# Kernel tuning notes

Hardware: AMD Instinct MI355X
Metric: run time of the kernel (lower is better)

## Reference

```python
import jax, jax.numpy as jnp
import numpy as np

N_NODES = 100000
N_EDGES = 1600000
NODE_IN = 6
EDGE_IN = 4
HID = 128


def _glorot(key, shape):
    fan_in, fan_out = shape[0], shape[1]
    lim = (6.0 / (fan_in + fan_out)) ** 0.5
    return jax.random.uniform(key, shape, jnp.float32, -lim, lim)


def setup_inputs() -> dict:
    key = jax.random.key(0)
    ks = jax.random.split(key, 16)
    x = jax.random.normal(ks[0], (N_NODES, NODE_IN), jnp.float32)
    edge_index = jax.random.randint(ks[1], (2, N_EDGES), 0, N_NODES, jnp.int64)
    edge_attr = jax.random.normal(ks[2], (N_EDGES, EDGE_IN), jnp.float32)
    # SAGEConv params: out = x @ W_root + mean_neigh @ W_neigh + b
    params = {
        "w1_root": _glorot(ks[3], (NODE_IN, HID)),
        "w1_neigh": _glorot(ks[4], (NODE_IN, HID)),
        "b1": jnp.zeros((HID,), jnp.float32),
        "w2_root": _glorot(ks[5], (HID, HID)),
        "w2_neigh": _glorot(ks[6], (HID, HID)),
        "b2": jnp.zeros((HID,), jnp.float32),
        "w_e1": _glorot(ks[7], (2 * HID + EDGE_IN, HID)),
        "b_e1": jnp.zeros((HID,), jnp.float32),
        "w_e2": _glorot(ks[8], (HID, HID // 2)),
        "b_e2": jnp.zeros((HID // 2,), jnp.float32),
        "w_e3": _glorot(ks[9], (HID // 2, 1)),
        "b_e3": jnp.zeros((1,), jnp.float32),
    }
    return {"x": x, "edge_index": edge_index, "edge_attr": edge_attr, **params}


def _sage(x, src, dst, w_root, w_neigh, b):
    # mean aggregation of source features into destination nodes
    agg = jax.ops.segment_sum(x[src], dst, num_segments=N_NODES)
    cnt = jax.ops.segment_sum(jnp.ones((src.shape[0], 1), x.dtype), dst, num_segments=N_NODES)
    mean = agg / jnp.maximum(cnt, 1.0)
    return x @ w_root + mean @ w_neigh + b


def reference(x, edge_index, edge_attr,
              w1_root, w1_neigh, b1, w2_root, w2_neigh, b2,
              w_e1, b_e1, w_e2, b_e2, w_e3, b_e3):
    src, dst = edge_index[0], edge_index[1]
    h = jax.nn.relu(_sage(x, src, dst, w1_root, w1_neigh, b1))
    # dropout is identity in eval mode
    h = jax.nn.relu(_sage(h, src, dst, w2_root, w2_neigh, b2))
    # per-edge representation: [h[src], h[dst], edge_attr] -> MLP -> scalar
    e = jnp.concatenate([h[src], h[dst], edge_attr], axis=-1)  # [E, 2H+Ein]
    e = jax.nn.relu(e @ w_e1 + b_e1)
    e = jax.nn.relu(e @ w_e2 + b_e2)
    out = (e @ w_e3 + b_e3).squeeze(-1)  # [E]
    return out
```

## Files before the change

kernel.cpp:

```cpp
#include <hip/hip_runtime.h>
#include <hip/hip_bf16.h>
#include <stdint.h>


typedef unsigned short u16;
typedef short bf16x8 __attribute__((ext_vector_type(8)));
typedef float f32x4 __attribute__((ext_vector_type(4)));

#define NMASK 0x1FFFF

__device__ __forceinline__ u16 f2b(float f) {
  unsigned u = __builtin_bit_cast(unsigned, f);
  u = u + 0x7fffu + ((u >> 16) & 1u);
  return (u16)(u >> 16);
}
__device__ __forceinline__ float bflo(unsigned u) {
  return __builtin_bit_cast(float, u << 16);
}
__device__ __forceinline__ float bfhi(unsigned u) {
  return __builtin_bit_cast(float, u & 0xffff0000u);
}
__device__ __forceinline__ unsigned pack2bf(float a, float b) {
  unsigned ua = __builtin_bit_cast(unsigned, a);
  unsigned ub = __builtin_bit_cast(unsigned, b);
  ua = ua + 0x7fffu + ((ua >> 16) & 1u);
  ub = ub + 0x7fffu + ((ub >> 16) & 1u);
  return (ua >> 16) | (ub & 0xffff0000u);
}

__global__ void hist_kernel(const int* __restrict__ ei, int* __restrict__ cnt,
                            int E) {
  int e = blockIdx.x * blockDim.x + threadIdx.x;
  if (e < E) atomicAdd(&cnt[ei[E + e]], 1);
}

__global__ void scan_block_sums(const int* __restrict__ cnt,
                                int* __restrict__ partial, int N) {
  __shared__ int red[256];
  int t = threadIdx.x;
  int n = blockIdx.x * 256 + t;
  red[t] = (n < N) ? cnt[n] : 0;
  __syncthreads();
  for (int off = 128; off; off >>= 1) {
    if (t < off) red[t] += red[t + off];
    __syncthreads();
  }
  if (t == 0) partial[blockIdx.x] = red[0];
}

__global__ void scan_partials(int* __restrict__ partial,
                              int* __restrict__ rowptr, int NBLK, int E,
                              int N) {
  __shared__ int sc[512];
  int t = threadIdx.x;
  int v = (t < NBLK) ? partial[t] : 0;
  sc[t] = v;
  __syncthreads();
  for (int off = 1; off < 512; off <<= 1) {
    int a = (t >= off) ? sc[t - off] : 0;
    __syncthreads();
    sc[t] += a;
    __syncthreads();
  }
  if (t < NBLK) partial[t] = sc[t] - v;
  if (t == 0) rowptr[N] = E;
}

__global__ void scan_final(const int* __restrict__ partial,
                           int* __restrict__ cursor, int* __restrict__ rowptr,
                           int N) {
  __shared__ int sc[256];
  int t = threadIdx.x;
  int n = blockIdx.x * 256 + t;
  int v = (n < N) ? cursor[n] : 0;
  sc[t] = v;
  __syncthreads();
  for (int off = 1; off < 256; off <<= 1) {
    int a = (t >= off) ? sc[t - off] : 0;
    __syncthreads();
    sc[t] += a;
    __syncthreads();
  }
  int excl = partial[blockIdx.x] + sc[t] - v;
  if (n < N) {
    rowptr[n] = excl;
    cursor[n] = excl;
  }
}

__global__ void scatter_csr(const int* __restrict__ ei,
                            int* __restrict__ cursor, uint2* __restrict__ csr2,
                            int E) {
  int e = blockIdx.x * blockDim.x + threadIdx.x;
  if (e >= E) return;
  int s = ei[e];
  int d = ei[E + e];
  int pos = atomicAdd(&cursor[d], 1);
  unsigned long long v = (unsigned long long)(unsigned)s |
                         ((unsigned long long)(unsigned)d << 17) |
                         ((unsigned long long)(unsigned)e << 34);
  csr2[pos] = make_uint2((unsigned)v, (unsigned)(v >> 32));
}

__global__ void permute_attr(const float* __restrict__ attr,
                             const uint2* __restrict__ csr2,
                             float4* __restrict__ attrp, int E) {
  int i = blockIdx.x * 256 + threadIdx.x;
  if (i >= E) return;
  uint2 pk = csr2[i];
  int eid = (int)((((unsigned long long)pk.y << 32) | pk.x) >> 34);
  attrp[i] = *(const float4*)(attr + (size_t)eid * 4);
}

__global__ void pack_weights(const float* __restrict__ w2_root,
                             const float* __restrict__ w2_neigh,
                             const float* __restrict__ w_e1,
                             const float* __restrict__ w_e2,
                             const float* __restrict__ b_e1,
                             u16* __restrict__ B2f, u16* __restrict__ WSDf,
                             u16* __restrict__ W2f, float* __restrict__ pbias) {
  int t = blockIdx.x * 256 + threadIdx.x;
  if (t < 32768) {
    int j = t & 7, lane = (t >> 3) & 63, nt = (t >> 9) & 7, kt = t >> 12;
    int k = kt * 32 + (lane >> 4) * 8 + j;
    int n = nt * 16 + (lane & 15);
    float v = (k < 128) ? w2_root[k * 128 + n] : w2_neigh[(k - 128) * 128 + n];
    B2f[t] = f2b(v);
  } else if (t < 65536) {
    int t2 = t - 32768;
    int j = t2 & 7, lane = (t2 >> 3) & 63, nt = (t2 >> 9) & 15, kt = t2 >> 13;
    int k = kt * 32 + (lane >> 4) * 8 + j;
    int n = nt * 16 + (lane & 15);
    float v = (n < 128) ? w_e1[k * 128 + n] : w_e1[(128 + k) * 128 + (n - 128)];
    WSDf[t2] = f2b(v);
  } else if (t < 73728) {
    int t2 = t - 65536;
    int j = t2 & 7, lane = (t2 >> 3) & 63, nt = (t2 >> 9) & 3, kt = t2 >> 11;
    int k = kt * 32 + (lane >> 4) * 8 + j;
    int n = nt * 16 + (lane & 15);
    W2f[t2] = f2b(w_e2[k * 64 + n]);
  } else if (t < 73984) {
    int n = t - 73728;
    pbias[n] = (n < 128) ? 0.0f : b_e1[n - 128];
  }
}

__global__ __launch_bounds__(256) void agg1_kernel(
    const float* __restrict__ x, const int* __restrict__ rowptr,
    const uint2* __restrict__ csr2, float* __restrict__ mean1, int N) {
  int n = blockIdx.x * 4 + (threadIdx.x >> 6);
  if (n >= N) return;
  int lane = threadIdx.x & 63;
  int g = lane >> 3;
  int c = lane & 7;
  int beg = rowptr[n], end = rowptr[n + 1];
  float a = 0.0f;
  if (c < 6) {
    for (int i = beg + g; i < end; i += 8) {
      int s = (int)(csr2[i].x & NMASK);
      a += x[(size_t)s * 6 + c];
    }
  }
  a += __shfl_xor(a, 8, 64);
  a += __shfl_xor(a, 16, 64);
  a += __shfl_xor(a, 32, 64);
  if (g == 0 && c < 6)
    mean1[(size_t)n * 6 + c] = a / (float)max(end - beg, 1);
}

__global__ void dense1_kernel(const float* __restrict__ x,
                              const float* __restrict__ mean1,
                              const float* __restrict__ w_root,
                              const float* __restrict__ w_neigh,
                              const float* __restrict__ b,
                              u16* __restrict__ cat2b, int N) {
  int n = blockIdx.x;
  int m = threadIdx.x;
  if (n >= N) return;
  float s = b[m];
#pragma unroll
  for (int j = 0; j < 6; j++) {
    s += x[(size_t)n * 6 + j] * w_root[j * 128 + m] +
         mean1[(size_t)n * 6 + j] * w_neigh[j * 128 + m];
  }
  cat2b[(size_t)n * 256 + m] = f2b(fmaxf(s, 0.0f));
}

__global__ __launch_bounds__(256) void agg2_kernel(
    const u16* __restrict__ cat2b, u16* __restrict__ cat2w,
    const int* __restrict__ rowptr, const uint2* __restrict__ csr2, int N) {
  int n = blockIdx.x * 4 + (threadIdx.x >> 6);
  if (n >= N) return;
  int lane = threadIdx.x & 63;
  int g = lane >> 4;
  int c = lane & 15;
  int beg = rowptr[n], end = rowptr[n + 1];
  float acc[8];
#pragma unroll
  for (int j = 0; j < 8; j++) acc[j] = 0.0f;
  for (int i = beg + g; i < end; i += 4) {
    int s = (int)(csr2[i].x & NMASK);
    uint4 u = *(const uint4*)(cat2b + (size_t)s * 256 + c * 8);
    acc[0] += bflo(u.x); acc[1] += bfhi(u.x);
    acc[2] += bflo(u.y); acc[3] += bfhi(u.y);
    acc[4] += bflo(u.z); acc[5] += bfhi(u.z);
    acc[6] += bflo(u.w); acc[7] += bfhi(u.w);
  }
#pragma unroll
  for (int j = 0; j < 8; j++) {
    acc[j] += __shfl_xor(acc[j], 16, 64);
    acc[j] += __shfl_xor(acc[j], 32, 64);
  }
  if (g == 0) {
    float inv = 1.0f / (float)max(end - beg, 1);
    uint4 ov;
    ov.x = pack2bf(acc[0] * inv, acc[1] * inv);
    ov.y = pack2bf(acc[2] * inv, acc[3] * inv);
    ov.z = pack2bf(acc[4] * inv, acc[5] * inv);
    ov.w = pack2bf(acc[6] * inv, acc[7] * inv);
    *(uint4*)(cat2w + (size_t)n * 256 + 128 + c * 8) = ov;
  }
}

template <int KT, int NT, bool RELU>
__global__ __launch_bounds__(256) void mfma_gemm(
    const u16* __restrict__ A, int lda, const u16* __restrict__ Bf,
    const float* __restrict__ bias, u16* __restrict__ C, int ldc, int M) {
  __shared__ u16 sB[KT * NT * 512];
  int tid = threadIdx.x;
  for (int i = tid; i < KT * NT * 64; i += 256)
    ((uint4*)sB)[i] = ((const uint4*)Bf)[i];
  int w = tid >> 6, l = tid & 63;
  int quad = l >> 4, col16 = l & 15;
  int rowA = blockIdx.x * 64 + w * 16 + col16;
  bool rv = rowA < M;
  const u16* ap = A + (size_t)rowA * lda + quad * 8;
  f32x4 acc[NT];
#pragma unroll
  for (int nt = 0; nt < NT; nt++) acc[nt] = (f32x4){0.f, 0.f, 0.f, 0.f};
  __syncthreads();
#pragma unroll
  for (int kt = 0; kt < KT; kt++) {
    bf16x8 av = {};
    if (rv) av = *(const bf16x8*)(ap + kt * 32);
#pragma unroll
    for (int nt = 0; nt < NT; nt++) {
      bf16x8 bv = *(const bf16x8*)(sB + ((kt * NT + nt) * 64 + l) * 8);
      acc[nt] = __builtin_amdgcn_mfma_f32_16x16x32_bf16(av, bv, acc[nt], 0, 0, 0);
    }
  }
  int rowbase = blockIdx.x * 64 + w * 16 + quad * 4;
#pragma unroll
  for (int r = 0; r < 4; r++) {
    int row = rowbase + r;
    if (row < M) {
#pragma unroll
      for (int nt = 0; nt < NT; nt++) {
        float v = acc[nt][r] + bias[nt * 16 + col16];
        if (RELU) v = fmaxf(v, 0.0f);
        C[(size_t)row * ldc + nt * 16 + col16] = f2b(v);
      }
    }
  }
}

__global__ __launch_bounds__(256) void edge_mfma_kernel(
    const u16* __restrict__ Pcatb, const uint2* __restrict__ csr2,
    const float4* __restrict__ attrp, const float* __restrict__ w_e1,
    const u16* __restrict__ W2f, const float* __restrict__ b_e2,
    const float* __restrict__ w_e3, const float* __restrict__ b_e3,
    float* __restrict__ out, int E) {
  __shared__ u16 sV[2][64 * 136];
  __shared__ u16 sW2[8192];

  int tid = threadIdx.x;
  int w = tid >> 6, l = tid & 63, quad = l >> 4, c16 = l & 15;
  int egrp = tid >> 4, ac16 = tid & 15;

  for (int i = tid; i < 1024; i += 256)
    ((uint4*)sW2)[i] = ((const uint4*)W2f)[i];

  float wa[4][8];
#pragma unroll
  for (int j = 0; j < 4; j++) {
    *(float4*)&wa[j][0] = *(const float4*)(w_e1 + (256 + j) * 128 + ac16 * 8);
    *(float4*)&wa[j][4] = *(const float4*)(w_e1 + (256 + j) * 128 + ac16 * 8 + 4);
  }
  float w3v[4], be2[4];
#pragma unroll
  for (int nt = 0; nt < 4; nt++) {
    w3v[nt] = w_e3[nt * 16 + c16];
    be2[nt] = b_e2[nt * 16 + c16];
  }
  float b3 = b_e3[0];

  int tiles = (E + 63) >> 6;
  int S = gridDim.x;

  uint2 pk[4];
  uint4 ps[4], pd[4];
  float4 at[4];
  int eidr[4];

  auto load_pk = [&](int t) {
#pragma unroll
    for (int it = 0; it < 4; it++) {
      int e = min(t * 64 + it * 16 + egrp, E - 1);
      pk[it] = csr2[e];
    }
  };
  auto issue_gather = [&](int t) {
#pragma unroll
    for (int it = 0; it < 4; it++) {
      unsigned long long v =
          ((unsigned long long)pk[it].y << 32) | pk[it].x;
      int s = (int)(v & NMASK);
      int d = (int)((v >> 17) & NMASK);
      eidr[it] = (int)(v >> 34);
      ps[it] = *(const uint4*)(Pcatb + (size_t)s * 256 + ac16 * 8);
      pd[it] = *(const uint4*)(Pcatb + (size_t)d * 256 + 128 + ac16 * 8);
      int e = min(t * 64 + it * 16 + egrp, E - 1);
      at[it] = attrp[e];
    }
  };

  int t = blockIdx.x;
  if (t < tiles) {
    load_pk(t);
    issue_gather(t);
    if (t + S < tiles) load_pk(t + S);
  }
  int buf = 0;
  for (; t < tiles; t += S) {
    u16* sv = sV[buf];
#pragma unroll
    for (int it = 0; it < 4; it++) {
      int e = it * 16 + egrp;
      uint4 psu = ps[it], pdu = pd[it];
      float4 a4 = at[it];
      unsigned pu[4] = {psu.x, psu.y, psu.z, psu.w};
      unsigned du[4] = {pdu.x, pdu.y, pdu.z, pdu.w};
      uint4 ov;
      unsigned* op = (unsigned*)&ov;
#pragma unroll
      for (int p2 = 0; p2 < 4; p2++) {
        int t0 = p2 * 2, t1 = t0 + 1;
        float f0 = bflo(pu[p2]) + bflo(du[p2]) + a4.x * wa[0][t0] +
                   a4.y * wa[1][t0] + a4.z * wa[2][t0] + a4.w * wa[3][t0];
        float f1 = bfhi(pu[p2]) + bfhi(du[p2]) + a4.x * wa[0][t1] +
                   a4.y * wa[1][t1] + a4.z * wa[2][t1] + a4.w * wa[3][t1];
        op[p2] = pack2bf(fmaxf(f0, 0.0f), fmaxf(f1, 0.0f));
      }
      *(uint4*)(sv + e * 136 + ac16 * 8) = ov;
      if (ac16 == 0) *(unsigned*)(sv + e * 136 + 128) = (unsigned)eidr[it];
    }
    if (t + S < tiles) {
      issue_gather(t + S);
      if (t + 2 * S < tiles) load_pk(t + 2 * S);
    }
    __syncthreads();
    f32x4 acc[4];
#pragma unroll
    for (int nt = 0; nt < 4; nt++) acc[nt] = (f32x4){0.f, 0.f, 0.f, 0.f};
    const u16* vp = sv + (w * 16 + c16) * 136 + quad * 8;
#pragma unroll
    for (int kt = 0; kt < 4; kt++) {
      bf16x8 av = *(const bf16x8*)(vp + kt * 32);
#pragma unroll
      for (int nt = 0; nt < 4; nt++) {
        bf16x8 bv = *(const bf16x8*)(sW2 + ((kt * 4 + nt) * 64 + l) * 8);
        acc[nt] = __builtin_amdgcn_mfma_f32_16x16x32_bf16(av, bv, acc[nt], 0, 0, 0);
      }
    }
#pragma unroll
    for (int r = 0; r < 4; r++) {
      float p = 0.0f;
#pragma unroll
      for (int nt = 0; nt < 4; nt++)
        p += fmaxf(acc[nt][r] + be2[nt], 0.0f) * w3v[nt];
      p += __shfl_xor(p, 1, 64);
      p += __shfl_xor(p, 2, 64);
      p += __shfl_xor(p, 4, 64);
      p += __shfl_xor(p, 8, 64);
      if (c16 == 0) {
        int eloc = w * 16 + quad * 4 + r;
        if (t * 64 + eloc < E) {
          unsigned eid = *(const unsigned*)(sv + eloc * 136 + 128);
          out[eid] = p + b3;
        }
      }
    }
    buf ^= 1;
  }
}

extern "C" void kernel_launch(void* const* d_in, const int* in_sizes, int n_in,
                              void* d_out, int out_size, void* d_ws,
                              size_t ws_size, hipStream_t stream) {
  const float* x        = (const float*)d_in[0];
  const int*   ei       = (const int*)d_in[1];
  const float* attr     = (const float*)d_in[2];
  const float* w1_root  = (const float*)d_in[3];
  const float* w1_neigh = (const float*)d_in[4];
  const float* b1       = (const float*)d_in[5];
  const float* w2_root  = (const float*)d_in[6];
  const float* w2_neigh = (const float*)d_in[7];
  const float* b2       = (const float*)d_in[8];
  const float* w_e1     = (const float*)d_in[9];
  const float* b_e1     = (const float*)d_in[10];
  const float* w_e2     = (const float*)d_in[11];
  const float* b_e2     = (const float*)d_in[12];
  const float* w_e3     = (const float*)d_in[13];
  const float* b_e3     = (const float*)d_in[14];
  float* out = (float*)d_out;

  int N = in_sizes[0] / 6;
  int E = in_sizes[2] / 4;
  int NBLK = (N + 255) / 256;

  int* wsi = (int*)d_ws;
  int*    rowptr  = wsi;
  int*    cursor  = wsi + 100004;
  int*    partial = wsi + 200004;
  uint2*  csr2    = (uint2*)(wsi + 200520);
  float*  mean1   = (float*)(wsi + 3400520);
  u16*    cat2b   = (u16*)(wsi + 4000520);
  u16*    h2b     = (u16*)(wsi + 16800520);
  u16*    B2f     = (u16*)(wsi + 23200520);
  u16*    WSDf    = (u16*)(wsi + 23216904);
  u16*    W2f     = (u16*)(wsi + 23233288);
  float*  pbias   = (float*)(wsi + 23237384);
  float4* attrp   = (float4*)(wsi + 23237640);

  hipMemsetAsync(cursor, 0, (size_t)N * sizeof(int), stream);

  pack_weights<<<289, 256, 0, stream>>>(w2_root, w2_neigh, w_e1, w_e2, b_e1,
                                        B2f, WSDf, W2f, pbias);

  hist_kernel<<<(E + 255) / 256, 256, 0, stream>>>(ei, cursor, E);
  scan_block_sums<<<NBLK, 256, 0, stream>>>(cursor, partial, N);
  scan_partials<<<1, 512, 0, stream>>>(partial, rowptr, NBLK, E, N);
  scan_final<<<NBLK, 256, 0, stream>>>(partial, cursor, rowptr, N);
  scatter_csr<<<(E + 255) / 256, 256, 0, stream>>>(ei, cursor, csr2, E);
  permute_attr<<<(E + 255) / 256, 256, 0, stream>>>(attr, csr2, attrp, E);

  agg1_kernel<<<(N + 3) / 4, 256, 0, stream>>>(x, rowptr, csr2, mean1, N);
  dense1_kernel<<<N, 128, 0, stream>>>(x, mean1, w1_root, w1_neigh, b1, cat2b, N);

  agg2_kernel<<<(N + 3) / 4, 256, 0, stream>>>(cat2b, cat2b, rowptr, csr2, N);

  int gblocks = (N + 63) / 64;
  mfma_gemm<8, 8, true><<<gblocks, 256, 0, stream>>>(cat2b, 256, B2f, b2, h2b,
                                                     128, N);
  mfma_gemm<4, 16, false><<<gblocks, 256, 0, stream>>>(h2b, 128, WSDf, pbias,
                                                       cat2b, 256, N);

  edge_mfma_kernel<<<1024, 256, 0, stream>>>(cat2b, csr2, attrp, w_e1, W2f,
                                             b_e2, w_e3, b_e3, out, E);
}
```

Before: 657.6 us.

## Fuse attr permutation into CSR scatter, prefetch agg2 gathers, pack f32x2 math

Result: faster. 612.0 us (-6.9%).

```diff
diff --git a/kernel.cpp b/kernel.cpp
--- a/kernel.cpp
+++ b/kernel.cpp
@@ -6,6 +6,7 @@
 typedef unsigned short u16;
 typedef short bf16x8 __attribute__((ext_vector_type(8)));
 typedef float f32x4 __attribute__((ext_vector_type(4)));
+typedef float f32x2 __attribute__((ext_vector_type(2)));
 
 #define NMASK 0x1FFFF
 
@@ -19,6 +20,9 @@
 }
 __device__ __forceinline__ float bfhi(unsigned u) {
   return __builtin_bit_cast(float, u & 0xffff0000u);
+}
+__device__ __forceinline__ f32x2 unpk2(unsigned u) {
+  return (f32x2){bflo(u), bfhi(u)};
 }
 __device__ __forceinline__ unsigned pack2bf(float a, float b) {
   unsigned ua = __builtin_bit_cast(unsigned, a);
@@ -89,27 +93,20 @@
 }
 
 __global__ void scatter_csr(const int* __restrict__ ei,
+                            const float* __restrict__ attr,
                             int* __restrict__ cursor, uint2* __restrict__ csr2,
-                            int E) {
+                            float4* __restrict__ attrp, int E) {
   int e = blockIdx.x * blockDim.x + threadIdx.x;
   if (e >= E) return;
   int s = ei[e];
   int d = ei[E + e];
+  float4 a4 = *(const float4*)(attr + (size_t)e * 4);
   int pos = atomicAdd(&cursor[d], 1);
   unsigned long long v = (unsigned long long)(unsigned)s |
                          ((unsigned long long)(unsigned)d << 17) |
                          ((unsigned long long)(unsigned)e << 34);
   csr2[pos] = make_uint2((unsigned)v, (unsigned)(v >> 32));
-}
-
-__global__ void permute_attr(const float* __restrict__ attr,
-                             const uint2* __restrict__ csr2,
-                             float4* __restrict__ attrp, int E) {
-  int i = blockIdx.x * 256 + threadIdx.x;
-  if (i >= E) return;
-  uint2 pk = csr2[i];
-  int eid = (int)((((unsigned long long)pk.y << 32) | pk.x) >> 34);
-  attrp[i] = *(const float4*)(attr + (size_t)eid * 4);
+  attrp[pos] = a4;
 }
 
 __global__ void pack_weights(const float* __restrict__ w2_root,
@@ -195,29 +192,44 @@
   int g = lane >> 4;
   int c = lane & 15;
   int beg = rowptr[n], end = rowptr[n + 1];
-  float acc[8];
-#pragma unroll
-  for (int j = 0; j < 8; j++) acc[j] = 0.0f;
-  for (int i = beg + g; i < end; i += 4) {
-    int s = (int)(csr2[i].x & NMASK);
-    uint4 u = *(const uint4*)(cat2b + (size_t)s * 256 + c * 8);
-    acc[0] += bflo(u.x); acc[1] += bfhi(u.x);
-    acc[2] += bflo(u.y); acc[3] += bfhi(u.y);
-    acc[4] += bflo(u.z); acc[5] += bfhi(u.z);
-    acc[6] += bflo(u.w); acc[7] += bfhi(u.w);
-  }
-#pragma unroll
-  for (int j = 0; j < 8; j++) {
-    acc[j] += __shfl_xor(acc[j], 16, 64);
-    acc[j] += __shfl_xor(acc[j], 32, 64);
+  f32x2 acc2[4];
+#pragma unroll
+  for (int j = 0; j < 4; j++) acc2[j] = (f32x2){0.f, 0.f};
+
+  int i = beg + g;
+  uint4 u0, u1;
+  bool h0 = i < end, h1 = (i + 4) < end;
+  if (h0)
+    u0 = *(const uint4*)(cat2b + (size_t)(csr2[i].x & NMASK) * 256 + c * 8);
+  if (h1)
+    u1 = *(const uint4*)(cat2b + (size_t)(csr2[i + 4].x & NMASK) * 256 + c * 8);
+  while (h0) {
+    uint4 uc = u0;
+    i += 4;
+    h0 = h1;
+    u0 = u1;
+    h1 = (i + 4) < end;
+    if (h1)
+      u1 = *(const uint4*)(cat2b + (size_t)(csr2[i + 4].x & NMASK) * 256 + c * 8);
+    acc2[0] += unpk2(uc.x);
+    acc2[1] += unpk2(uc.y);
+    acc2[2] += unpk2(uc.z);
+    acc2[3] += unpk2(uc.w);
+  }
+#pragma unroll
+  for (int j = 0; j < 4; j++) {
+    acc2[j].x += __shfl_xor(acc2[j].x, 16, 64);
+    acc2[j].y += __shfl_xor(acc2[j].y, 16, 64);
+    acc2[j].x += __shfl_xor(acc2[j].x, 32, 64);
+    acc2[j].y += __shfl_xor(acc2[j].y, 32, 64);
   }
   if (g == 0) {
     float inv = 1.0f / (float)max(end - beg, 1);
     uint4 ov;
-    ov.x = pack2bf(acc[0] * inv, acc[1] * inv);
-    ov.y = pack2bf(acc[2] * inv, acc[3] * inv);
-    ov.z = pack2bf(acc[4] * inv, acc[5] * inv);
-    ov.w = pack2bf(acc[6] * inv, acc[7] * inv);
+    ov.x = pack2bf(acc2[0].x * inv, acc2[0].y * inv);
+    ov.y = pack2bf(acc2[1].x * inv, acc2[1].y * inv);
+    ov.z = pack2bf(acc2[2].x * inv, acc2[2].y * inv);
+    ov.w = pack2bf(acc2[3].x * inv, acc2[3].y * inv);
     *(uint4*)(cat2w + (size_t)n * 256 + 128 + c * 8) = ov;
   }
 }
@@ -280,11 +292,15 @@
   for (int i = tid; i < 1024; i += 256)
     ((uint4*)sW2)[i] = ((const uint4*)W2f)[i];
 
-  float wa[4][8];
+  f32x2 wa2[4][4];
 #pragma unroll
   for (int j = 0; j < 4; j++) {
-    *(float4*)&wa[j][0] = *(const float4*)(w_e1 + (256 + j) * 128 + ac16 * 8);
-    *(float4*)&wa[j][4] = *(const float4*)(w_e1 + (256 + j) * 128 + ac16 * 8 + 4);
+    float4 w0 = *(const float4*)(w_e1 + (256 + j) * 128 + ac16 * 8);
+    float4 w1 = *(const float4*)(w_e1 + (256 + j) * 128 + ac16 * 8 + 4);
+    wa2[j][0] = (f32x2){w0.x, w0.y};
+    wa2[j][1] = (f32x2){w0.z, w0.w};
+    wa2[j][2] = (f32x2){w1.x, w1.y};
+    wa2[j][3] = (f32x2){w1.z, w1.w};
   }
   float w3v[4], be2[4];
 #pragma unroll
@@ -312,8 +328,7 @@
   auto issue_gather = [&](int t) {
 #pragma unroll
     for (int it = 0; it < 4; it++) {
-      unsigned long long v =
-          ((unsigned long long)pk[it].y << 32) | pk[it].x;
+      unsigned long long v = ((unsigned long long)pk[it].y << 32) | pk[it].x;
       int s = (int)(v & NMASK);
       int d = (int)((v >> 17) & NMASK);
       eidr[it] = (int)(v >> 34);
@@ -344,12 +359,13 @@
       unsigned* op = (unsigned*)&ov;
 #pragma unroll
       for (int p2 = 0; p2 < 4; p2++) {
-        int t0 = p2 * 2, t1 = t0 + 1;
-        float f0 = bflo(pu[p2]) + bflo(du[p2]) + a4.x * wa[0][t0] +
-                   a4.y * wa[1][t0] + a4.z * wa[2][t0] + a4.w * wa[3][t0];
-        float f1 = bfhi(pu[p2]) + bfhi(du[p2]) + a4.x * wa[0][t1] +
-                   a4.y * wa[1][t1] + a4.z * wa[2][t1] + a4.w * wa[3][t1];
-        op[p2] = pack2bf(fmaxf(f0, 0.0f), fmaxf(f1, 0.0f));
+        f32x2 f = unpk2(pu[p2]) + unpk2(du[p2]);
+        f += a4.x * wa2[0][p2];
+        f += a4.y * wa2[1][p2];
+        f += a4.z * wa2[2][p2];
+        f += a4.w * wa2[3][p2];
+        f = __builtin_elementwise_max(f, (f32x2){0.f, 0.f});
+        op[p2] = pack2bf(f.x, f.y);
       }
       *(uint4*)(sv + e * 136 + ac16 * 8) = ov;
       if (ac16 == 0) *(unsigned*)(sv + e * 136 + 128) = (unsigned)eidr[it];
@@ -362,7 +378,7 @@
     f32x4 acc[4];
 #pragma unroll
     for (int nt = 0; nt < 4; nt++) acc[nt] = (f32x4){0.f, 0.f, 0.f, 0.f};
-    const u16* vp = sv + (w * 16 + c16) * 136 + quad * 8;
+    const u16* vp = sV[buf] + (w * 16 + c16) * 136 + quad * 8;
 #pragma unroll
     for (int kt = 0; kt < 4; kt++) {
       bf16x8 av = *(const bf16x8*)(vp + kt * 32);
@@ -385,7 +401,7 @@
       if (c16 == 0) {
         int eloc = w * 16 + quad * 4 + r;
         if (t * 64 + eloc < E) {
-          unsigned eid = *(const unsigned*)(sv + eloc * 136 + 128);
+          unsigned eid = *(const unsigned*)(sV[buf] + eloc * 136 + 128);
           out[eid] = p + b3;
         }
       }
@@ -441,8 +457,8 @@
   scan_block_sums<<<NBLK, 256, 0, stream>>>(cursor, partial, N);
   scan_partials<<<1, 512, 0, stream>>>(partial, rowptr, NBLK, E, N);
   scan_final<<<NBLK, 256, 0, stream>>>(partial, cursor, rowptr, N);
-  scatter_csr<<<(E + 255) / 256, 256, 0, stream>>>(ei, cursor, csr2, E);
-  permute_attr<<<(E + 255) / 256, 256, 0, stream>>>(attr, csr2, attrp, E);
+  scatter_csr<<<(E + 255) / 256, 256, 0, stream>>>(ei, attr, cursor, csr2,
+                                                   attrp, E);
 
   agg1_kernel<<<(N + 3) / 4, 256, 0, stream>>>(x, rowptr, csr2, mean1, N);
   dense1_kernel<<<N, 128, 0, stream>>>(x, mean1, w1_root, w1_neigh, b1, cat2b, N);
```
